# Performance work log

Measured on AMD Instinct MI355X. Metric: run time of the kernel, lower is better.

Reference implementation:

```python
import jax, jax.numpy as jnp
import numpy as np

# ---- config (matches init_kwargs) ----
DIM = 1024
HEADS = 8            # local_heads == heads
QK_HD = 128          # qk_head_dim
V_HD = 128           # v_head_dim
NOPE = 64            # qk_nope_head_dim
ROPE = 64            # qk_rope_head_dim
KV_LORA = 256
N_EXP = 32
N_GROUPS = 8
TOPK = 4             # n_activated_experts
TOPK_GROUPS = 4
INTER = 512
N_SHARED = 1
ROUTE_SCALE = 1.0
EPS = 1e-6


def rmsnorm(x, w):
    xf = x.astype(jnp.float32)
    rms = jnp.sqrt(jnp.mean(xf ** 2, axis=-1, keepdims=True) + EPS)
    return (xf / rms * w).astype(x.dtype)


def setup_inputs() -> dict:
    key = jax.random.key(0)
    ks = jax.random.split(key, 16)
    s = 0.02
    return {
        "x": jax.random.normal(ks[0], (2, 1024, DIM), jnp.float32),
        # attention sub-layer params
        "norm_attn": jnp.ones((DIM,), jnp.float32),
        "wq": jax.random.normal(ks[1], (DIM, HEADS * QK_HD), jnp.float32) * s,
        "wkv_a": jax.random.normal(ks[2], (DIM, KV_LORA + ROPE), jnp.float32) * s,
        "kv_norm_w": jnp.ones((KV_LORA,), jnp.float32),
        "wkv_b": jax.random.normal(ks[3], (KV_LORA, HEADS * (NOPE + V_HD)), jnp.float32) * s,
        "wo": jax.random.normal(ks[4], (HEADS * V_HD, DIM), jnp.float32) * s,
        # MoE sub-layer params
        "norm_moe": jnp.ones((DIM,), jnp.float32),
        "gate_w": jax.random.normal(ks[5], (N_EXP, DIM), jnp.float32) * 0.01,
        "gate_b": jnp.zeros((N_EXP,), jnp.float32),
        "ew1": jax.random.normal(ks[6], (N_EXP, DIM, INTER), jnp.float32) * s,
        "ew2": jax.random.normal(ks[7], (N_EXP, INTER, DIM), jnp.float32) * s,
        "ew3": jax.random.normal(ks[8], (N_EXP, DIM, INTER), jnp.float32) * s,
        "sw1": jax.random.normal(ks[9], (DIM, N_SHARED * INTER), jnp.float32) * s,
        "sw2": jax.random.normal(ks[10], (N_SHARED * INTER, DIM), jnp.float32) * s,
        "sw3": jax.random.normal(ks[11], (DIM, N_SHARED * INTER), jnp.float32) * s,
    }


def _mla(x, wq, wkv_a, kv_norm_w, wkv_b, wo):
    B, S, _ = x.shape
    # q_lora_rank == 0 -> direct q projection; nope/rope split+concat is identity
    q = (x @ wq).reshape(B, S, HEADS, QK_HD)
    kv = x @ wkv_a                                   # [B,S,KV_LORA+ROPE]
    c, k_pe = kv[..., :KV_LORA], kv[..., KV_LORA:]
    kvp = (rmsnorm(c, kv_norm_w) @ wkv_b).reshape(B, S, HEADS, NOPE + V_HD)
    k_nope, v = kvp[..., :NOPE], kvp[..., NOPE:]
    k = jnp.concatenate(
        [k_nope, jnp.broadcast_to(k_pe[:, :, None, :], (B, S, HEADS, ROPE))], axis=-1)
    out = jax.nn.dot_product_attention(q, k, v, scale=QK_HD ** -0.5, is_causal=True)
    return out.reshape(B, S, -1) @ wo


def _gate(xf, gate_w, gate_b):
    T = xf.shape[0]
    scores = jax.nn.sigmoid(xf @ gate_w.T)           # [T,E]
    original = scores
    s = scores + gate_b
    # hierarchical group selection: top-2 score sum per group, keep top groups
    sg = s.reshape(T, N_GROUPS, -1)
    group_score = jnp.sort(sg, axis=-1)[..., -2:].sum(axis=-1)
    group_idx = jnp.argsort(group_score, axis=-1)[..., -TOPK_GROUPS:]
    mask = jnp.ones((T, N_GROUPS), bool).at[jnp.arange(T)[:, None], group_idx].set(False)
    s = jnp.where(mask[..., None], -jnp.inf, sg).reshape(T, -1)
    indices = jnp.argsort(s, axis=-1)[..., -TOPK:]   # [T,K]
    w = jnp.take_along_axis(original, indices, axis=1)
    w = w / (w.sum(axis=-1, keepdims=True) + 1e-20)  # sigmoid normalization
    return w * ROUTE_SCALE, indices


def _moe(xf, gate_w, gate_b, ew1, ew2, ew3, sw1, sw2, sw3):
    # dense all-expert SwiGLU as in the original (nn.vmap over axis_size=E)
    weights, indices = _gate(xf, gate_w, gate_b)
    h = jax.nn.silu(jnp.einsum('td,edh->eth', xf, ew1)) * jnp.einsum('td,edh->eth', xf, ew3)
    all_out = jnp.einsum('eth,ehd->etd', h, ew2)     # [E,T,dim]
    # per-token gather of its top-k experts, weighted combine
    selected = jnp.take_along_axis(all_out.transpose(1, 0, 2), indices[:, :, None], axis=1)  # [T,K,dim]
    y = (selected * weights[..., None]).sum(axis=1)
    z = (jax.nn.silu(xf @ sw1) * (xf @ sw3)) @ sw2   # shared expert MLP
    return y + z


def reference(x, norm_attn, wq, wkv_a, kv_norm_w, wkv_b, wo,
              norm_moe, gate_w, gate_b, ew1, ew2, ew3, sw1, sw2, sw3):
    # MLA layer: x + MLA(RMSNorm(x))
    x = x + _mla(rmsnorm(x, norm_attn), wq, wkv_a, kv_norm_w, wkv_b, wo)
    # MoE layer: x + MoE(RMSNorm(x))
    shape = x.shape
    xf = rmsnorm(x, norm_moe).reshape(-1, DIM)
    y = _moe(xf, gate_w, gate_b, ew1, ew2, ew3, sw1, sw2, sw3)
    return x + y.reshape(shape)
```

## Files before the change

### kernel.cpp

```cpp
#include <hip/hip_runtime.h>
#include <hip/hip_bf16.h>

#define T_TOK 2048
#define DIM 1024
#define HEADS 8
#define QK_HD 128
#define V_HD 128
#define NOPE 64
#define ROPE 64
#define KV_LORA 256
#define N_EXP 32
#define TOPK 4
#define INTER 512
#define S_LEN 1024
#define KVP_W (HEADS * (NOPE + V_HD))

typedef __attribute__((ext_vector_type(8))) _Float16 f16x8;
typedef __attribute__((ext_vector_type(4))) float f32x4;

__device__ inline unsigned short f2h(float f) {
  union { _Float16 h; unsigned short u; } c;
  c.h = (_Float16)f;
  return c.u;
}
__device__ inline float h2f(unsigned short u) {
  union { _Float16 h; unsigned short u; } c;
  c.u = u;
  return (float)c.h;
}

__launch_bounds__(256)
__global__ void tcvt_k(const float* __restrict__ src, unsigned short* __restrict__ dst,
                       int K, int N) {
  int e = blockIdx.z;
  src += (size_t)e * K * N;
  dst += (size_t)e * K * N;
  int n0 = blockIdx.x * 32, k0 = blockIdx.y * 32;
  __shared__ float ts[32][33];
  int tid = threadIdx.x;
  int r = tid >> 3, c4 = (tid & 7) * 4;
  float4 v = *(const float4*)(src + (size_t)(k0 + r) * N + n0 + c4);
  ts[r][c4] = v.x; ts[r][c4 + 1] = v.y; ts[r][c4 + 2] = v.z; ts[r][c4 + 3] = v.w;
  __syncthreads();
  ushort4 o;
  o.x = f2h(ts[c4][r]);
  o.y = f2h(ts[c4 + 1][r]);
  o.z = f2h(ts[c4 + 2][r]);
  o.w = f2h(ts[c4 + 3][r]);
  *(ushort4*)(dst + (size_t)(n0 + r) * K + k0 + c4) = o;
}

__launch_bounds__(64)
__global__ void zero_counters_k(int* __restrict__ counts, int* __restrict__ fill) {
  int i = threadIdx.x;
  if (i < N_EXP) { counts[i] = 0; fill[i] = 0; }
}

__launch_bounds__(256)
__global__ void rmsnorm_k(const float* __restrict__ x, int in_stride, int width,
                          const float* __restrict__ w, unsigned short* __restrict__ out,
                          float* __restrict__ out2, int out_stride) {
  int row = blockIdx.x;
  const float* xr = x + (size_t)row * in_stride;
  float ss = 0.f;
  for (int i = threadIdx.x; i < width; i += 256) { float v = xr[i]; ss += v * v; }
  #pragma unroll
  for (int off = 32; off; off >>= 1) ss += __shfl_down(ss, off, 64);
  __shared__ float red[4];
  if ((threadIdx.x & 63) == 0) red[threadIdx.x >> 6] = ss;
  __syncthreads();
  if (threadIdx.x == 0) {
    float tot = red[0] + red[1] + red[2] + red[3];
    red[0] = rsqrtf(tot / (float)width + 1e-6f);
  }
  __syncthreads();
  float scale = red[0];
  for (int i = threadIdx.x; i < width; i += 256) {
    float v = xr[i] * scale * w[i];
    out[(size_t)row * out_stride + i] = f2h(v);
    if (out2) out2[(size_t)row * out_stride + i] = v;
  }
}

template <int RES, int OUTH>
__launch_bounds__(256)
__global__ void gemm_bt_k(const unsigned short* __restrict__ A,
                          const unsigned short* __restrict__ B,
                          const float* __restrict__ R, void* __restrict__ Cout,
                          int N, int K) {
  const int n0 = blockIdx.x * 64;
  const int m0 = blockIdx.y * 64;
  __shared__ __align__(16) unsigned short As[64][72];
  __shared__ __align__(16) unsigned short Bs[64][72];
  const int tid = threadIdx.x;
  const int lane = tid & 63, wave = tid >> 6;
  const int quad = lane >> 4, lm = lane & 15;
  const int wm = (wave >> 1) * 32, wn = (wave & 1) * 32;
  f32x4 acc[2][2] = {};
  const int sr = tid >> 2, sc = tid & 3;
  const unsigned short* Ap = A + (size_t)(m0 + sr) * K;
  const unsigned short* Bp = B + (size_t)(n0 + sr) * K;
  for (int k0 = 0; k0 < K; k0 += 64) {
    f16x8 a0 = *(const f16x8*)(Ap + k0 + sc * 8);
    f16x8 a1 = *(const f16x8*)(Ap + k0 + sc * 8 + 32);
    f16x8 b0 = *(const f16x8*)(Bp + k0 + sc * 8);
    f16x8 b1 = *(const f16x8*)(Bp + k0 + sc * 8 + 32);
    __syncthreads();
    *(f16x8*)&As[sr][sc * 8] = a0;
    *(f16x8*)&As[sr][sc * 8 + 32] = a1;
    *(f16x8*)&Bs[sr][sc * 8] = b0;
    *(f16x8*)&Bs[sr][sc * 8 + 32] = b1;
    __syncthreads();
    #pragma unroll
    for (int ks = 0; ks < 2; ks++) {
      f16x8 af0 = *(const f16x8*)&As[wm + lm][ks * 32 + quad * 8];
      f16x8 af1 = *(const f16x8*)&As[wm + 16 + lm][ks * 32 + quad * 8];
      f16x8 bf0 = *(const f16x8*)&Bs[wn + lm][ks * 32 + quad * 8];
      f16x8 bf1 = *(const f16x8*)&Bs[wn + 16 + lm][ks * 32 + quad * 8];
      acc[0][0] = __builtin_amdgcn_mfma_f32_16x16x32_f16(af0, bf0, acc[0][0], 0, 0, 0);
      acc[0][1] = __builtin_amdgcn_mfma_f32_16x16x32_f16(af0, bf1, acc[0][1], 0, 0, 0);
      acc[1][0] = __builtin_amdgcn_mfma_f32_16x16x32_f16(af1, bf0, acc[1][0], 0, 0, 0);
      acc[1][1] = __builtin_amdgcn_mfma_f32_16x16x32_f16(af1, bf1, acc[1][1], 0, 0, 0);
    }
  }
  #pragma unroll
  for (int i = 0; i < 2; i++)
    #pragma unroll
    for (int j = 0; j < 2; j++) {
      int row = m0 + wm + i * 16 + quad * 4;
      int col = n0 + wn + j * 16 + lm;
      #pragma unroll
      for (int r = 0; r < 4; r++) {
        float v = acc[i][j][r];
        if (RES) v += R[(size_t)(row + r) * N + col];
        if (OUTH) ((unsigned short*)Cout)[(size_t)(row + r) * N + col] = f2h(v);
        else ((float*)Cout)[(size_t)(row + r) * N + col] = v;
      }
    }
}

__launch_bounds__(256)
__global__ void moe_up_k(const unsigned short* __restrict__ xfb,
                         const unsigned short* __restrict__ w1t,
                         const unsigned short* __restrict__ w3t,
                         unsigned short* __restrict__ hout,
                         const int* __restrict__ perm, const int* __restrict__ offs,
                         int Mfull) {
  const int e = blockIdx.z;
  int base = 0, count = Mfull;
  if (offs) { base = offs[e]; count = offs[e + 1] - base; }
  const int m0 = blockIdx.y * 64;
  if (m0 >= count) return;
  const int n0 = blockIdx.x * 64;
  const unsigned short* W1 = w1t + (size_t)e * (INTER * DIM);
  const unsigned short* W3 = w3t + (size_t)e * (INTER * DIM);
  __shared__ __align__(16) unsigned short As[64][72];
  __shared__ __align__(16) unsigned short B1s[64][72];
  __shared__ __align__(16) unsigned short B2s[64][72];
  __shared__ int toks[64];
  const int tid = threadIdx.x;
  if (tid < 64) {
    int g = m0 + tid;
    toks[tid] = (g < count) ? (perm ? (perm[base + g] >> 2) : g) : -1;
  }
  __syncthreads();
  const int lane = tid & 63, wave = tid >> 6;
  const int quad = lane >> 4, lm = lane & 15;
  const int wm = (wave >> 1) * 32, wn = (wave & 1) * 32;
  f32x4 acc1[2][2] = {};
  f32x4 acc2[2][2] = {};
  const int sr = tid >> 2, sc = tid & 3;
  const int tok = toks[sr];
  const unsigned short* Ap = xfb + (size_t)(tok < 0 ? 0 : tok) * DIM;
  const bool av = (tok >= 0);
  const unsigned short* B1p = W1 + (size_t)(n0 + sr) * DIM;
  const unsigned short* B2p = W3 + (size_t)(n0 + sr) * DIM;
  for (int k0 = 0; k0 < DIM; k0 += 64) {
    f16x8 a0 = {0,0,0,0,0,0,0,0}, a1 = {0,0,0,0,0,0,0,0};
    if (av) {
      a0 = *(const f16x8*)(Ap + k0 + sc * 8);
      a1 = *(const f16x8*)(Ap + k0 + sc * 8 + 32);
    }
    f16x8 b10 = *(const f16x8*)(B1p + k0 + sc * 8);
    f16x8 b11 = *(const f16x8*)(B1p + k0 + sc * 8 + 32);
    f16x8 b20 = *(const f16x8*)(B2p + k0 + sc * 8);
    f16x8 b21 = *(const f16x8*)(B2p + k0 + sc * 8 + 32);
    __syncthreads();
    *(f16x8*)&As[sr][sc * 8] = a0;
    *(f16x8*)&As[sr][sc * 8 + 32] = a1;
    *(f16x8*)&B1s[sr][sc * 8] = b10;
    *(f16x8*)&B1s[sr][sc * 8 + 32] = b11;
    *(f16x8*)&B2s[sr][sc * 8] = b20;
    *(f16x8*)&B2s[sr][sc * 8 + 32] = b21;
    __syncthreads();
    #pragma unroll
    for (int ks = 0; ks < 2; ks++) {
      f16x8 af0 = *(const f16x8*)&As[wm + lm][ks * 32 + quad * 8];
      f16x8 af1 = *(const f16x8*)&As[wm + 16 + lm][ks * 32 + quad * 8];
      f16x8 b1f0 = *(const f16x8*)&B1s[wn + lm][ks * 32 + quad * 8];
      f16x8 b1f1 = *(const f16x8*)&B1s[wn + 16 + lm][ks * 32 + quad * 8];
      f16x8 b2f0 = *(const f16x8*)&B2s[wn + lm][ks * 32 + quad * 8];
      f16x8 b2f1 = *(const f16x8*)&B2s[wn + 16 + lm][ks * 32 + quad * 8];
      acc1[0][0] = __builtin_amdgcn_mfma_f32_16x16x32_f16(af0, b1f0, acc1[0][0], 0, 0, 0);
      acc1[0][1] = __builtin_amdgcn_mfma_f32_16x16x32_f16(af0, b1f1, acc1[0][1], 0, 0, 0);
      acc1[1][0] = __builtin_amdgcn_mfma_f32_16x16x32_f16(af1, b1f0, acc1[1][0], 0, 0, 0);
      acc1[1][1] = __builtin_amdgcn_mfma_f32_16x16x32_f16(af1, b1f1, acc1[1][1], 0, 0, 0);
      acc2[0][0] = __builtin_amdgcn_mfma_f32_16x16x32_f16(af0, b2f0, acc2[0][0], 0, 0, 0);
      acc2[0][1] = __builtin_amdgcn_mfma_f32_16x16x32_f16(af0, b2f1, acc2[0][1], 0, 0, 0);
      acc2[1][0] = __builtin_amdgcn_mfma_f32_16x16x32_f16(af1, b2f0, acc2[1][0], 0, 0, 0);
      acc2[1][1] = __builtin_amdgcn_mfma_f32_16x16x32_f16(af1, b2f1, acc2[1][1], 0, 0, 0);
    }
  }
  #pragma unroll
  for (int i = 0; i < 2; i++)
    #pragma unroll
    for (int j = 0; j < 2; j++) {
      int col = n0 + wn + j * 16 + lm;
      #pragma unroll
      for (int r = 0; r < 4; r++) {
        int g = m0 + wm + i * 16 + quad * 4 + r;
        if (g < count) {
          float u = acc1[i][j][r];
          float vv = acc2[i][j][r];
          float h = (u / (1.f + __expf(-u))) * vv;
          hout[(size_t)(base + g) * INTER + col] = f2h(h);
        }
      }
    }
}

__launch_bounds__(256)
__global__ void moe_down_k(const unsigned short* __restrict__ hbuf,
                           const unsigned short* __restrict__ w2t,
                           unsigned short* __restrict__ dout,
                           const int* __restrict__ offs, int Mfull) {
  const int e = blockIdx.z;
  int base = 0, count = Mfull;
  if (offs) { base = offs[e]; count = offs[e + 1] - base; }
  const int m0 = blockIdx.y * 64;
  if (m0 >= count) return;
  const int n0 = blockIdx.x * 64;
  const unsigned short* W2 = w2t + (size_t)e * (DIM * INTER);
  __shared__ __align__(16) unsigned short As[64][72];
  __shared__ __align__(16) unsigned short Bs[64][72];
  const int tid = threadIdx.x;
  const int lane = tid & 63, wave = tid >> 6;
  const int quad = lane >> 4, lm = lane & 15;
  const int wm = (wave >> 1) * 32, wn = (wave & 1) * 32;
  f32x4 acc[2][2] = {};
  const int sr = tid >> 2, sc = tid & 3;
  const int g_s = m0 + sr;
  const bool av = (g_s < count);
  const unsigned short* Ap = hbuf + (size_t)(base + (av ? g_s : 0)) * INTER;
  const unsigned short* Bp = W2 + (size_t)(n0 + sr) * INTER;
  for (int k0 = 0; k0 < INTER; k0 += 64) {
    f16x8 a0 = {0,0,0,0,0,0,0,0}, a1 = {0,0,0,0,0,0,0,0};
    if (av) {
      a0 = *(const f16x8*)(Ap + k0 + sc * 8);
      a1 = *(const f16x8*)(Ap + k0 + sc * 8 + 32);
    }
    f16x8 b0 = *(const f16x8*)(Bp + k0 + sc * 8);
    f16x8 b1 = *(const f16x8*)(Bp + k0 + sc * 8 + 32);
    __syncthreads();
    *(f16x8*)&As[sr][sc * 8] = a0;
    *(f16x8*)&As[sr][sc * 8 + 32] = a1;
    *(f16x8*)&Bs[sr][sc * 8] = b0;
    *(f16x8*)&Bs[sr][sc * 8 + 32] = b1;
    __syncthreads();
    #pragma unroll
    for (int ks = 0; ks < 2; ks++) {
      f16x8 af0 = *(const f16x8*)&As[wm + lm][ks * 32 + quad * 8];
      f16x8 af1 = *(const f16x8*)&As[wm + 16 + lm][ks * 32 + quad * 8];
      f16x8 bf0 = *(const f16x8*)&Bs[wn + lm][ks * 32 + quad * 8];
      f16x8 bf1 = *(const f16x8*)&Bs[wn + 16 + lm][ks * 32 + quad * 8];
      acc[0][0] = __builtin_amdgcn_mfma_f32_16x16x32_f16(af0, bf0, acc[0][0], 0, 0, 0);
      acc[0][1] = __builtin_amdgcn_mfma_f32_16x16x32_f16(af0, bf1, acc[0][1], 0, 0, 0);
      acc[1][0] = __builtin_amdgcn_mfma_f32_16x16x32_f16(af1, bf0, acc[1][0], 0, 0, 0);
      acc[1][1] = __builtin_amdgcn_mfma_f32_16x16x32_f16(af1, bf1, acc[1][1], 0, 0, 0);
    }
  }
  #pragma unroll
  for (int i = 0; i < 2; i++)
    #pragma unroll
    for (int j = 0; j < 2; j++) {
      int col = n0 + wn + j * 16 + lm;
      #pragma unroll
      for (int r = 0; r < 4; r++) {
        int g = m0 + wm + i * 16 + quad * 4 + r;
        if (g < count)
          dout[(size_t)(base + g) * DIM + col] = f2h(acc[i][j][r]);
      }
    }
}

__launch_bounds__(256)
__global__ void attn_k(const unsigned short* __restrict__ q,
                       const unsigned short* __restrict__ kvp,
                       const float* __restrict__ kvb,
                       unsigned short* __restrict__ o) {
  const int qt = blockIdx.x, h = blockIdx.y, b = blockIdx.z;
  __shared__ __align__(16) _Float16 Qs[64][136];
  __shared__ __align__(16) _Float16 Ks[64][136];
  __shared__ __align__(16) _Float16 Vt[128][72];
  __shared__ __align__(16) _Float16 Ps[4][16][72];
  const int tid = threadIdx.x;
  const int lane = tid & 63, wave = tid >> 6;
  const int quad = lane >> 4, lm = lane & 15;
  const int qr0 = wave * 16;
  const float scale = 0.08838834764831845f;
  const int tq = b * S_LEN + qt * 64;

  for (int i = tid; i < 64 * 16; i += 256) {
    int row = i & 63, g = i >> 6;
    *(f16x8*)&Qs[row][g * 8] =
        *(const f16x8*)(q + (size_t)(tq + row) * 1024 + h * 128 + g * 8);
  }

  float m_i[4], l_i[4];
  #pragma unroll
  for (int r = 0; r < 4; r++) { m_i[r] = -1e30f; l_i[r] = 0.f; }
  f32x4 o_acc[8] = {};

  for (int kt = 0; kt <= qt; ++kt) {
    const int tk = b * S_LEN + kt * 64;
    for (int i = tid; i < 64 * 8; i += 256) {
      int key = i & 63, g = i >> 6;
      *(f16x8*)&Ks[key][g * 8] =
          *(const f16x8*)(kvp + (size_t)(tk + key) * KVP_W + h * 192 + g * 8);
    }
    for (int i = tid; i < 64 * 16; i += 256) {
      int key = i & 63, g = i >> 6;
      float4 v = *(const float4*)(kvb + (size_t)(tk + key) * 320 + 256 + g * 4);
      ushort4 u;
      u.x = f2h(v.x); u.y = f2h(v.y); u.z = f2h(v.z); u.w = f2h(v.w);
      *(ushort4*)&Ks[key][64 + g * 4] = u;
    }
    for (int i = tid; i < 64 * 16; i += 256) {
      int key = i & 63, g = i >> 6;
      f16x8 v = *(const f16x8*)(kvp + (size_t)(tk + key) * KVP_W + h * 192 + 64 + g * 8);
      #pragma unroll
      for (int j = 0; j < 8; j++) Vt[g * 8 + j][key] = v[j];
    }
    __syncthreads();

    f32x4 sacc[4] = {};
    #pragma unroll
    for (int kc = 0; kc < 4; kc++) {
      f16x8 af = *(const f16x8*)&Qs[qr0 + lm][kc * 32 + quad * 8];
      #pragma unroll
      for (int jn = 0; jn < 4; jn++) {
        f16x8 bf = *(const f16x8*)&Ks[jn * 16 + lm][kc * 32 + quad * 8];
        sacc[jn] = __builtin_amdgcn_mfma_f32_16x16x32_f16(af, bf, sacc[jn], 0, 0, 0);
      }
    }
    const bool diag = (kt == qt);
    float p[4][4];
    float rowmax[4], rowsum[4];
    #pragma unroll
    for (int r = 0; r < 4; r++) rowmax[r] = -1e30f;
    #pragma unroll
    for (int jn = 0; jn < 4; jn++)
      #pragma unroll
      for (int r = 0; r < 4; r++) {
        float s = sacc[jn][r] * scale;
        if (diag && (jn * 16 + lm > qr0 + quad * 4 + r)) s = -1e30f;
        p[jn][r] = s;
        rowmax[r] = fmaxf(rowmax[r], s);
      }
    #pragma unroll
    for (int m = 1; m < 16; m <<= 1)
      #pragma unroll
      for (int r = 0; r < 4; r++)
        rowmax[r] = fmaxf(rowmax[r], __shfl_xor(rowmax[r], m, 64));
    float al[4];
    #pragma unroll
    for (int r = 0; r < 4; r++) {
      float mn = fmaxf(m_i[r], rowmax[r]);
      al[r] = __expf(m_i[r] - mn);
      m_i[r] = mn;
      rowsum[r] = 0.f;
    }
    #pragma unroll
    for (int jn = 0; jn < 4; jn++)
      #pragma unroll
      for (int r = 0; r < 4; r++) {
        float pv = __expf(p[jn][r] - m_i[r]);
        p[jn][r] = pv;
        rowsum[r] += pv;
      }
    #pragma unroll
    for (int m = 1; m < 16; m <<= 1)
      #pragma unroll
      for (int r = 0; r < 4; r++)
        rowsum[r] += __shfl_xor(rowsum[r], m, 64);
    #pragma unroll
    for (int r = 0; r < 4; r++) l_i[r] = l_i[r] * al[r] + rowsum[r];
    #pragma unroll
    for (int jn2 = 0; jn2 < 8; jn2++)
      #pragma unroll
      for (int r = 0; r < 4; r++) o_acc[jn2][r] *= al[r];
    #pragma unroll
    for (int jn = 0; jn < 4; jn++)
      #pragma unroll
      for (int r = 0; r < 4; r++)
        Ps[wave][quad * 4 + r][jn * 16 + lm] = (_Float16)p[jn][r];
    #pragma unroll
    for (int kc = 0; kc < 2; kc++) {
      f16x8 af = *(const f16x8*)&Ps[wave][lm][kc * 32 + quad * 8];
      #pragma unroll
      for (int jn2 = 0; jn2 < 8; jn2++) {
        f16x8 bf = *(const f16x8*)&Vt[jn2 * 16 + lm][kc * 32 + quad * 8];
        o_acc[jn2] = __builtin_amdgcn_mfma_f32_16x16x32_f16(af, bf, o_acc[jn2], 0, 0, 0);
      }
    }
    __syncthreads();
  }
  #pragma unroll
  for (int r = 0; r < 4; r++) l_i[r] = 1.f / l_i[r];
  #pragma unroll
  for (int jn2 = 0; jn2 < 8; jn2++) {
    int col = h * 128 + jn2 * 16 + lm;
    #pragma unroll
    for (int r = 0; r < 4; r++) {
      int row = tq + qr0 + quad * 4 + r;
      o[(size_t)row * 1024 + col] = f2h(o_acc[jn2][r] * l_i[r]);
    }
  }
}

__launch_bounds__(256)
__global__ void scores_k(const float* __restrict__ xf, const float* __restrict__ gw,
                         float* __restrict__ sc) {
  __shared__ float xls[32][129];
  __shared__ float gls[32][129];
  const int t0 = blockIdx.x * 32;
  const int tid = threadIdx.x;
  const int lr = tid >> 3, lc = tid & 7;
  const int e = tid & 31, tg = tid >> 5;
  float acc[4] = {};
  for (int k0 = 0; k0 < DIM; k0 += 128) {
    __syncthreads();
    #pragma unroll
    for (int it = 0; it < 4; it++) {
      int col = lc * 4 + it * 32;
      *(float4*)&xls[lr][col] = *(const float4*)(xf + (size_t)(t0 + lr) * DIM + k0 + col);
      *(float4*)&gls[lr][col] = *(const float4*)(gw + (size_t)lr * DIM + k0 + col);
    }
    __syncthreads();
    for (int d = 0; d < 128; d++) {
      float g = gls[e][d];
      #pragma unroll
      for (int j = 0; j < 4; j++)
        acc[j] += xls[tg * 4 + j][d] * g;
    }
  }
  #pragma unroll
  for (int j = 0; j < 4; j++)
    sc[(size_t)(t0 + tg * 4 + j) * N_EXP + e] = acc[j];
}

__launch_bounds__(64)
__global__ void route_k(const float* __restrict__ sc, const float* __restrict__ gb,
                        float* __restrict__ tw, int* __restrict__ tidx,
                        int* __restrict__ counts) {
  int t = blockIdx.x * 64 + threadIdx.x;
  if (t >= T_TOK) return;
  float orig[N_EXP], sb[N_EXP];
  #pragma unroll
  for (int i = 0; i < N_EXP; i++) {
    float s = 1.f / (1.f + __expf(-sc[(size_t)t * N_EXP + i]));
    orig[i] = s;
    sb[i] = s + gb[i];
  }
  float gsc[8];
  #pragma unroll
  for (int g = 0; g < 8; g++) {
    float m1 = -1e30f, m2 = -1e30f;
    #pragma unroll
    for (int j = 0; j < 4; j++) {
      float v = sb[g * 4 + j];
      if (v > m1) { m2 = m1; m1 = v; } else if (v > m2) m2 = v;
    }
    gsc[g] = m1 + m2;
  }
  unsigned gok = 0;
  #pragma unroll
  for (int it = 0; it < 4; it++) {
    int best = 0; float bv = -1e30f;
    #pragma unroll
    for (int g = 0; g < 8; g++)
      if (!((gok >> g) & 1u) && gsc[g] >= bv) { bv = gsc[g]; best = g; }
    gok |= 1u << best;
  }
  unsigned emask = 0;
  #pragma unroll
  for (int g = 0; g < 8; g++)
    if ((gok >> g) & 1u) emask |= 0xFu << (g * 4);
  unsigned taken = 0;
  int idx[TOPK]; float ow[TOPK]; float wsum = 0.f;
  #pragma unroll
  for (int k = 0; k < TOPK; k++) {
    int best = 0; float bv = -1e30f, bo = 0.f;
    #pragma unroll
    for (int i = 0; i < N_EXP; i++)
      if (((emask >> i) & 1u) && !((taken >> i) & 1u) && sb[i] >= bv) {
        bv = sb[i]; best = i; bo = orig[i];
      }
    taken |= 1u << best;
    idx[k] = best; ow[k] = bo; wsum += bo;
  }
  float inv = 1.f / (wsum + 1e-20f);
  #pragma unroll
  for (int k = 0; k < TOPK; k++) {
    tidx[t * TOPK + k] = idx[k];
    tw[t * TOPK + k] = ow[k] * inv;
    atomicAdd(&counts[idx[k]], 1);
  }
}

__global__ void scan_k(const int* __restrict__ counts, int* __restrict__ offs) {
  if (threadIdx.x == 0 && blockIdx.x == 0) {
    int acc = 0;
    for (int e = 0; e < N_EXP; e++) { offs[e] = acc; acc += counts[e]; }
    offs[N_EXP] = acc;
  }
}

__launch_bounds__(256)
__global__ void scatter_k(const int* __restrict__ tidx, const int* __restrict__ offs,
                          int* __restrict__ fill, int* __restrict__ perm,
                          int* __restrict__ posOf) {
  int t = blockIdx.x * 256 + threadIdx.x;
  if (t >= T_TOK) return;
  for (int j = 0; j < TOPK; j++) {
    int e = tidx[t * TOPK + j];
    int pos = atomicAdd(&fill[e], 1);
    int p = offs[e] + pos;
    perm[p] = t * TOPK + j;
    posOf[t * TOPK + j] = p;
  }
}

__launch_bounds__(256)
__global__ void final_gather_k(const float* __restrict__ x1,
                               const unsigned short* __restrict__ dbuf,
                               const unsigned short* __restrict__ sdbuf,
                               const int* __restrict__ posOf,
                               const float* __restrict__ tw,
                               float* __restrict__ out) {
  int t = blockIdx.x;
  int c0 = threadIdx.x * 4;
  int p0 = posOf[t * 4 + 0], p1 = posOf[t * 4 + 1];
  int p2 = posOf[t * 4 + 2], p3 = posOf[t * 4 + 3];
  float w0 = tw[t * 4 + 0], w1 = tw[t * 4 + 1];
  float w2 = tw[t * 4 + 2], w3 = tw[t * 4 + 3];
  size_t tb = (size_t)t * DIM;
  #pragma unroll
  for (int i = 0; i < 4; i++) {
    int c = c0 + i;
    float v = x1[tb + c] + h2f(sdbuf[tb + c])
            + w0 * h2f(dbuf[(size_t)p0 * DIM + c])
            + w1 * h2f(dbuf[(size_t)p1 * DIM + c])
            + w2 * h2f(dbuf[(size_t)p2 * DIM + c])
            + w3 * h2f(dbuf[(size_t)p3 * DIM + c]);
    out[tb + c] = v;
  }
}

extern "C" void kernel_launch(void* const* d_in, const int* in_sizes, int n_in,
                              void* d_out, int out_size, void* d_ws, size_t ws_size,
                              hipStream_t stream) {
  const float* x        = (const float*)d_in[0];
  const float* norm_attn= (const float*)d_in[1];
  const float* wq       = (const float*)d_in[2];
  const float* wkv_a    = (const float*)d_in[3];
  const float* kv_norm_w= (const float*)d_in[4];
  const float* wkv_b    = (const float*)d_in[5];
  const float* wo       = (const float*)d_in[6];
  const float* norm_moe = (const float*)d_in[7];
  const float* gate_w   = (const float*)d_in[8];
  const float* gate_b   = (const float*)d_in[9];
  const float* ew1      = (const float*)d_in[10];
  const float* ew2      = (const float*)d_in[11];
  const float* ew3      = (const float*)d_in[12];
  const float* sw1      = (const float*)d_in[13];
  const float* sw2      = (const float*)d_in[14];
  const float* sw3      = (const float*)d_in[15];
  float* out = (float*)d_out;

  char* wp = (char*)d_ws;
  auto alloc = [&](size_t bytes) -> char* {
    char* r = wp;
    wp += (bytes + 255) & ~(size_t)255;
    return r;
  };
  typedef unsigned short us;
  us* wqT   = (us*)alloc(1048576 * 2);
  us* wkvaT = (us*)alloc(327680 * 2);
  us* wkvbT = (us*)alloc(393216 * 2);
  us* woT   = (us*)alloc(1048576 * 2);
  us* ew1T  = (us*)alloc((size_t)16777216 * 2);
  us* ew3T  = (us*)alloc((size_t)16777216 * 2);
  us* ew2T  = (us*)alloc((size_t)16777216 * 2);
  us* sw1T  = (us*)alloc(524288 * 2);
  us* sw3T  = (us*)alloc(524288 * 2);
  us* sw2T  = (us*)alloc(524288 * 2);
  us* xb    = (us*)alloc(2097152 * 2);
  us* cn    = (us*)alloc(524288 * 2);
  us* atn   = (us*)alloc(2097152 * 2);
  us* dbuf  = (us*)alloc((size_t)8388608 * 2);
  us* qb    = (us*)alloc(2097152 * 4);
  float* kvb  = (float*)alloc(655360 * 4);
  us* kvp   = (us*)alloc(3145728 * 4);
  float* x1   = (float*)alloc(2097152 * 4);
  float* xf32 = (float*)alloc(2097152 * 4);
  float* scb  = (float*)alloc(65536 * 4);
  float* twb  = (float*)alloc(8192 * 4);
  int* tidx   = (int*)alloc(8192 * 4);
  int* perm   = (int*)alloc(8192 * 4);
  int* posOf  = (int*)alloc(8192 * 4);
  int* counts = (int*)alloc(64 * 4);
  int* offs   = (int*)alloc(64 * 4);
  int* fill   = (int*)alloc(64 * 4);
  us* sdbuf = qb;
  us* hbuf  = kvp;
  us* hs    = hbuf + (size_t)8192 * 512;

  tcvt_k<<<dim3(32, 32, 1), 256, 0, stream>>>(wq, wqT, 1024, 1024);
  tcvt_k<<<dim3(10, 32, 1), 256, 0, stream>>>(wkv_a, wkvaT, 1024, 320);
  tcvt_k<<<dim3(48, 8, 1), 256, 0, stream>>>(wkv_b, wkvbT, 256, 1536);
  tcvt_k<<<dim3(32, 32, 1), 256, 0, stream>>>(wo, woT, 1024, 1024);
  tcvt_k<<<dim3(16, 32, 32), 256, 0, stream>>>(ew1, ew1T, 1024, 512);
  tcvt_k<<<dim3(16, 32, 32), 256, 0, stream>>>(ew3, ew3T, 1024, 512);
  tcvt_k<<<dim3(32, 16, 32), 256, 0, stream>>>(ew2, ew2T, 512, 1024);
  tcvt_k<<<dim3(16, 32, 1), 256, 0, stream>>>(sw1, sw1T, 1024, 512);
  tcvt_k<<<dim3(16, 32, 1), 256, 0, stream>>>(sw3, sw3T, 1024, 512);
  tcvt_k<<<dim3(32, 16, 1), 256, 0, stream>>>(sw2, sw2T, 512, 1024);

  rmsnorm_k<<<T_TOK, 256, 0, stream>>>(x, DIM, DIM, norm_attn, xb, nullptr, DIM);
  gemm_bt_k<0, 1><<<dim3(16, 32), 256, 0, stream>>>(xb, wqT, nullptr, qb, 1024, 1024);
  gemm_bt_k<0, 0><<<dim3(5, 32), 256, 0, stream>>>(xb, wkvaT, nullptr, kvb, 320, 1024);
  rmsnorm_k<<<T_TOK, 256, 0, stream>>>(kvb, 320, KV_LORA, kv_norm_w, cn, nullptr, KV_LORA);
  gemm_bt_k<0, 1><<<dim3(24, 32), 256, 0, stream>>>(cn, wkvbT, nullptr, kvp, 1536, 256);
  attn_k<<<dim3(S_LEN / 64, HEADS, 2), 256, 0, stream>>>(qb, kvp, kvb, atn);
  gemm_bt_k<1, 0><<<dim3(16, 32), 256, 0, stream>>>(atn, woT, x, x1, 1024, 1024);

  rmsnorm_k<<<T_TOK, 256, 0, stream>>>(x1, DIM, DIM, norm_moe, xb, xf32, DIM);
  zero_counters_k<<<1, 64, 0, stream>>>(counts, fill);
  scores_k<<<T_TOK / 32, 256, 0, stream>>>(xf32, gate_w, scb);
  route_k<<<T_TOK / 64, 64, 0, stream>>>(scb, gate_b, twb, tidx, counts);
  scan_k<<<1, 1, 0, stream>>>(counts, offs);
  scatter_k<<<(T_TOK + 255) / 256, 256, 0, stream>>>(tidx, offs, fill, perm, posOf);
  moe_up_k<<<dim3(8, 32, 32), 256, 0, stream>>>(xb, ew1T, ew3T, hbuf, perm, offs, 0);
  moe_down_k<<<dim3(16, 32, 32), 256, 0, stream>>>(hbuf, ew2T, dbuf, offs, 0);
  moe_up_k<<<dim3(8, 32, 1), 256, 0, stream>>>(xb, sw1T, sw3T, hs, nullptr, nullptr, T_TOK);
  moe_down_k<<<dim3(16, 32, 1), 256, 0, stream>>>(hs, sw2T, sdbuf, nullptr, T_TOK);

  final_gather_k<<<T_TOK, 256, 0, stream>>>(x1, dbuf, sdbuf, posOf, twb, out);
}
```

Measured before the change: 582.4 us.

## Split causal attention over KV chunks with combine pass and pre-transposed V

Attention is split-K: each block handles up to 4 KV tiles for a query tile and writes unnormalized partial outputs plus running max and sum. A combine kernel then merges the partials with log-sum-exp rescaling. The split is meant to fix load imbalance and the low block count of the causal loop. A separate kernel pre-transposes V so the attention kernel can load it with vector reads instead of scattered LDS writes, and Q is kept in registers rather than LDS. In exchange it adds two launches, fp32 partial-output traffic, and reorders the expert-weight conversions so their buffer can be reused as scratch.

Result: faster. 564.7 us (-3.0%).

```diff
diff --git a/kernel.cpp b/kernel.cpp
--- a/kernel.cpp
+++ b/kernel.cpp
@@ -294,12 +294,31 @@
 }
 
 __launch_bounds__(256)
-__global__ void attn_k(const unsigned short* __restrict__ q,
-                       const unsigned short* __restrict__ kvp,
-                       const float* __restrict__ kvb,
-                       unsigned short* __restrict__ o) {
-  const int qt = blockIdx.x, h = blockIdx.y, b = blockIdx.z;
-  __shared__ __align__(16) _Float16 Qs[64][136];
+__global__ void vtrans_k(const unsigned short* __restrict__ kvp,
+                         unsigned short* __restrict__ vT) {
+  const int z = blockIdx.z, h = z & 7, b = z >> 3;
+  const int s0 = blockIdx.x * 32, d0 = blockIdx.y * 32;
+  __shared__ unsigned short ts[32][36];
+  const int tid = threadIdx.x;
+  const int r = tid >> 3, c4 = (tid & 7) * 4;
+  ushort4 v = *(const ushort4*)(kvp + (size_t)(b * S_LEN + s0 + r) * KVP_W + h * 192 + 64 + d0 + c4);
+  ts[r][c4] = v.x; ts[r][c4 + 1] = v.y; ts[r][c4 + 2] = v.z; ts[r][c4 + 3] = v.w;
+  __syncthreads();
+  ushort4 o;
+  o.x = ts[c4][r]; o.y = ts[c4 + 1][r]; o.z = ts[c4 + 2][r]; o.w = ts[c4 + 3][r];
+  *(ushort4*)(vT + ((size_t)z * 128 + d0 + r) * S_LEN + s0 + c4) = o;
+}
+
+__launch_bounds__(256)
+__global__ void attn_part_k(const unsigned short* __restrict__ q,
+                            const unsigned short* __restrict__ kvp,
+                            const float* __restrict__ kvb,
+                            const unsigned short* __restrict__ vT,
+                            float* __restrict__ opart, float* __restrict__ ml) {
+  const int qt = blockIdx.x, ch = blockIdx.y, z = blockIdx.z;
+  const int kt0 = ch * 4;
+  if (kt0 > qt) return;
+  const int h = z & 7, b = z >> 3;
   __shared__ __align__(16) _Float16 Ks[64][136];
   __shared__ __align__(16) _Float16 Vt[128][72];
   __shared__ __align__(16) _Float16 Ps[4][16][72];
@@ -310,18 +329,18 @@
   const float scale = 0.08838834764831845f;
   const int tq = b * S_LEN + qt * 64;
 
-  for (int i = tid; i < 64 * 16; i += 256) {
-    int row = i & 63, g = i >> 6;
-    *(f16x8*)&Qs[row][g * 8] =
-        *(const f16x8*)(q + (size_t)(tq + row) * 1024 + h * 128 + g * 8);
-  }
+  f16x8 qf[4];
+  #pragma unroll
+  for (int kc = 0; kc < 4; kc++)
+    qf[kc] = *(const f16x8*)(q + (size_t)(tq + qr0 + lm) * 1024 + h * 128 + kc * 32 + quad * 8);
 
   float m_i[4], l_i[4];
   #pragma unroll
   for (int r = 0; r < 4; r++) { m_i[r] = -1e30f; l_i[r] = 0.f; }
   f32x4 o_acc[8] = {};
 
-  for (int kt = 0; kt <= qt; ++kt) {
+  const int kt_end = (kt0 + 3 < qt) ? (kt0 + 3) : qt;
+  for (int kt = kt0; kt <= kt_end; ++kt) {
     const int tk = b * S_LEN + kt * 64;
     for (int i = tid; i < 64 * 8; i += 256) {
       int key = i & 63, g = i >> 6;
@@ -335,22 +354,20 @@
       u.x = f2h(v.x); u.y = f2h(v.y); u.z = f2h(v.z); u.w = f2h(v.w);
       *(ushort4*)&Ks[key][64 + g * 4] = u;
     }
-    for (int i = tid; i < 64 * 16; i += 256) {
-      int key = i & 63, g = i >> 6;
-      f16x8 v = *(const f16x8*)(kvp + (size_t)(tk + key) * KVP_W + h * 192 + 64 + g * 8);
-      #pragma unroll
-      for (int j = 0; j < 8; j++) Vt[g * 8 + j][key] = v[j];
+    for (int i = tid; i < 128 * 8; i += 256) {
+      int d = i >> 3, seg = i & 7;
+      *(f16x8*)&Vt[d][seg * 8] =
+          *(const f16x8*)(vT + ((size_t)z * 128 + d) * S_LEN + kt * 64 + seg * 8);
     }
     __syncthreads();
 
     f32x4 sacc[4] = {};
     #pragma unroll
     for (int kc = 0; kc < 4; kc++) {
-      f16x8 af = *(const f16x8*)&Qs[qr0 + lm][kc * 32 + quad * 8];
       #pragma unroll
       for (int jn = 0; jn < 4; jn++) {
         f16x8 bf = *(const f16x8*)&Ks[jn * 16 + lm][kc * 32 + quad * 8];
-        sacc[jn] = __builtin_amdgcn_mfma_f32_16x16x32_f16(af, bf, sacc[jn], 0, 0, 0);
+        sacc[jn] = __builtin_amdgcn_mfma_f32_16x16x32_f16(qf[kc], bf, sacc[jn], 0, 0, 0);
       }
     }
     const bool diag = (kt == qt);
@@ -415,16 +432,68 @@
     }
     __syncthreads();
   }
-  #pragma unroll
-  for (int r = 0; r < 4; r++) l_i[r] = 1.f / l_i[r];
+
+  const size_t slot = ((size_t)z * 16 + qt) * 4 + ch;
+  float* op = opart + slot * 8192;
   #pragma unroll
   for (int jn2 = 0; jn2 < 8; jn2++) {
-    int col = h * 128 + jn2 * 16 + lm;
+    int col = jn2 * 16 + lm;
     #pragma unroll
     for (int r = 0; r < 4; r++) {
-      int row = tq + qr0 + quad * 4 + r;
-      o[(size_t)row * 1024 + col] = f2h(o_acc[jn2][r] * l_i[r]);
-    }
+      int row = qr0 + quad * 4 + r;
+      op[(size_t)row * 128 + col] = o_acc[jn2][r];
+    }
+  }
+  if (lm == 0) {
+    #pragma unroll
+    for (int r = 0; r < 4; r++) {
+      int row = qr0 + quad * 4 + r;
+      ml[slot * 128 + row * 2] = m_i[r];
+      ml[slot * 128 + row * 2 + 1] = l_i[r];
+    }
+  }
+}
+
+__launch_bounds__(256)
+__global__ void attn_comb_k(const float* __restrict__ opart, const float* __restrict__ ml,
+                            unsigned short* __restrict__ o) {
+  const int qt = blockIdx.x, z = blockIdx.y;
+  const int h = z & 7, b = z >> 3;
+  const int nch = (qt >> 2) + 1;
+  const int tid = threadIdx.x;
+  const int colg = tid & 31;
+  const int tq = b * S_LEN + qt * 64;
+  const size_t slotbase = ((size_t)z * 16 + qt) * 4;
+  for (int row = tid >> 5; row < 64; row += 8) {
+    float mmax = -1e30f;
+    #pragma unroll
+    for (int c = 0; c < 4; c++)
+      if (c < nch) mmax = fmaxf(mmax, ml[(slotbase + c) * 128 + row * 2]);
+    float w[4];
+    float lsum = 0.f;
+    #pragma unroll
+    for (int c = 0; c < 4; c++) {
+      if (c < nch) {
+        float mc = ml[(slotbase + c) * 128 + row * 2];
+        float lc = ml[(slotbase + c) * 128 + row * 2 + 1];
+        w[c] = __expf(mc - mmax);
+        lsum += lc * w[c];
+      } else w[c] = 0.f;
+    }
+    float inv = 1.f / lsum;
+    float ax = 0.f, ay = 0.f, az = 0.f, aw = 0.f;
+    #pragma unroll
+    for (int c = 0; c < 4; c++) {
+      if (c < nch) {
+        const float* op = opart + (slotbase + c) * 8192 + (size_t)row * 128 + colg * 4;
+        float4 v = *(const float4*)op;
+        ax += w[c] * v.x; ay += w[c] * v.y; az += w[c] * v.z; aw += w[c] * v.w;
+      }
+    }
+    ushort4 u;
+    u.x = f2h(ax * inv); u.y = f2h(ay * inv);
+    u.z = f2h(az * inv); u.w = f2h(aw * inv);
+    *(ushort4*)(o + (size_t)(tq + row) * 1024 + h * 128 + colg * 4) = u;
   }
 }
 
@@ -622,28 +691,34 @@
   int* counts = (int*)alloc(64 * 4);
   int* offs   = (int*)alloc(64 * 4);
   int* fill   = (int*)alloc(64 * 4);
+  us* vT     = (us*)alloc((size_t)2 * 8 * 128 * 1024 * 2);
+  float* mlb = (float*)alloc((size_t)1024 * 128 * 4);
   us* sdbuf = qb;
   us* hbuf  = kvp;
   us* hs    = hbuf + (size_t)8192 * 512;
+  float* opart = (float*)ew1T;
 
   tcvt_k<<<dim3(32, 32, 1), 256, 0, stream>>>(wq, wqT, 1024, 1024);
   tcvt_k<<<dim3(10, 32, 1), 256, 0, stream>>>(wkv_a, wkvaT, 1024, 320);
   tcvt_k<<<dim3(48, 8, 1), 256, 0, stream>>>(wkv_b, wkvbT, 256, 1536);
   tcvt_k<<<dim3(32, 32, 1), 256, 0, stream>>>(wo, woT, 1024, 1024);
+
+  rmsnorm_k<<<T_TOK, 256, 0, stream>>>(x, DIM, DIM, norm_attn, xb, nullptr, DIM);
+  gemm_bt_k<0, 1><<<dim3(16, 32), 256, 0, stream>>>(xb, wqT, nullptr, qb, 1024, 1024);
+  gemm_bt_k<0, 0><<<dim3(5, 32), 256, 0, stream>>>(xb, wkvaT, nullptr, kvb, 320, 1024);
+  rmsnorm_k<<<T_TOK, 256, 0, stream>>>(kvb, 320, KV_LORA, kv_norm_w, cn, nullptr, KV_LORA);
+  gemm_bt_k<0, 1><<<dim3(24, 32), 256, 0, stream>>>(cn, wkvbT, nullptr, kvp, 1536, 256);
+  vtrans_k<<<dim3(32, 4, 16), 256, 0, stream>>>(kvp, vT);
+  attn_part_k<<<dim3(16, 4, 16), 256, 0, stream>>>(qb, kvp, kvb, vT, opart, mlb);
+  attn_comb_k<<<dim3(16, 16), 256, 0, stream>>>(opart, mlb, atn);
+  gemm_bt_k<1, 0><<<dim3(16, 32), 256, 0, stream>>>(atn, woT, x, x1, 1024, 1024);
+
   tcvt_k<<<dim3(16, 32, 32), 256, 0, stream>>>(ew1, ew1T, 1024, 512);
   tcvt_k<<<dim3(16, 32, 32), 256, 0, stream>>>(ew3, ew3T, 1024, 512);
   tcvt_k<<<dim3(32, 16, 32), 256, 0, stream>>>(ew2, ew2T, 512, 1024);
   tcvt_k<<<dim3(16, 32, 1), 256, 0, stream>>>(sw1, sw1T, 1024, 512);
   tcvt_k<<<dim3(16, 32, 1), 256, 0, stream>>>(sw3, sw3T, 1024, 512);
   tcvt_k<<<dim3(32, 16, 1), 256, 0, stream>>>(sw2, sw2T, 512, 1024);
-
-  rmsnorm_k<<<T_TOK, 256, 0, stream>>>(x, DIM, DIM, norm_attn, xb, nullptr, DIM);
-  gemm_bt_k<0, 1><<<dim3(16, 32), 256, 0, stream>>>(xb, wqT, nullptr, qb, 1024, 1024);
-  gemm_bt_k<0, 0><<<dim3(5, 32), 256, 0, stream>>>(xb, wkvaT, nullptr, kvb, 320, 1024);
-  rmsnorm_k<<<T_TOK, 256, 0, stream>>>(kvb, 320, KV_LORA, kv_norm_w, cn, nullptr, KV_LORA);
-  gemm_bt_k<0, 1><<<dim3(24, 32), 256, 0, stream>>>(cn, wkvbT, nullptr, kvp, 1536, 256);
-  attn_k<<<dim3(S_LEN / 64, HEADS, 2), 256, 0, stream>>>(qb, kvp, kvb, atn);
-  gemm_bt_k<1, 0><<<dim3(16, 32), 256, 0, stream>>>(atn, woT, x, x1, 1024, 1024);
 
   rmsnorm_k<<<T_TOK, 256, 0, stream>>>(x1, DIM, DIM, norm_moe, xb, xf32, DIM);
   zero_counters_k<<<1, 64, 0, stream>>>(counts, fill);
```
